# Optimization experiments

Hardware: AMD Instinct MI355X
Metric: run time of the kernel (lower is better)

## Reference

```python
import jax, jax.numpy as jnp
import numpy as np

N_QUBITS = 14
N_LAYERS = 2
BATCH = 512


def _apply_ry(state, theta, wire):
    # state: [B, 2,...,2] (n_qubits axes of size 2); theta: [B] per-sample angle
    c = jnp.cos(theta * 0.5)[:, None]
    s = jnp.sin(theta * 0.5)[:, None]
    st = jnp.moveaxis(state, wire + 1, 1)
    shp = st.shape
    st = st.reshape(shp[0], 2, -1)
    a0, a1 = st[:, 0], st[:, 1]
    # RY = [[cos, -sin], [sin, cos]] (real matrix, so the state stays real)
    st = jnp.stack([c * a0 - s * a1, s * a0 + c * a1], axis=1)
    return jnp.moveaxis(st.reshape(shp), 1, wire + 1)


def _apply_cnot(state, ctrl, tgt):
    ca, ta = ctrl + 1, tgt + 1
    s0 = jnp.take(state, 0, axis=ca)
    s1 = jnp.take(state, 1, axis=ca)
    # flip target axis on the control=1 slice (axis index shifts if it was after ctrl)
    s1 = jnp.flip(s1, axis=ta if ta < ca else ta - 1)
    return jnp.stack([s0, s1], axis=ca)


def _circuit(x, weights):
    B, n = x.shape
    L = weights.shape[0]
    # |0...0> initial state, batched
    state = jnp.zeros((B,) + (2,) * n, x.dtype).at[(slice(None),) + (0,) * n].set(1.0)
    # angle encoding: RY(x[b, w]) on wire w
    for w in range(n):
        state = _apply_ry(state, x[:, w], w)
    # BasicEntanglerLayers: per layer, RY(weights[l, w]) on each wire, then CNOT ring
    for l in range(L):
        for w in range(n):
            state = _apply_ry(state, jnp.broadcast_to(weights[l, w], (B,)), w)
        for w in range(n):
            state = _apply_cnot(state, w, (w + 1) % n)
    # <Z_w> = P(bit_w = 0) - P(bit_w = 1)
    probs = state * state
    exps = []
    for w in range(n):
        p = jnp.moveaxis(probs, w + 1, 1).reshape(B, 2, -1).sum(-1)
        exps.append(p[:, 0] - p[:, 1])
    return jnp.stack(exps, axis=1)  # [B, n_qubits]


def setup_inputs() -> dict:
    key = jax.random.key(0)
    k1, k2 = jax.random.split(key)
    x = jax.random.normal(k1, (BATCH, N_QUBITS), dtype=jnp.float32)
    weights = (2.0 * np.pi) * jax.random.uniform(k2, (N_LAYERS, N_QUBITS), dtype=jnp.float32)
    return {"x": x, "weights": weights}


def reference(x, weights):
    return _circuit(x, weights)
```

## Files before the change

### kernel.cpp

```cpp
#include <hip/hip_runtime.h>

#define NQ 14
#define BLOCK 256
#define NG 28

typedef float f32x2 __attribute__((ext_vector_type(2)));
__device__ __forceinline__ f32x2 mk2(float a, float b) { f32x2 r; r.x = a; r.y = b; return r; }

struct Sched { unsigned m[NG]; unsigned r[NG]; unsigned fr[NQ]; };

constexpr Sched build_sched() {
  Sched sc{};
  unsigned col[NQ] = {}, rowinv[NQ] = {};
  for (int p = 0; p < NQ; ++p) { col[p] = 1u << p; rowinv[p] = 1u << p; }
  int g = 0;
  for (int l = 0; l < 2; ++l) {
    for (int w = 0; w < NQ; ++w) { int p = NQ - 1 - w; sc.m[g] = col[p]; sc.r[g] = rowinv[p]; ++g; }
    for (int w = 0; w < NQ; ++w) {
      int tgt = (w + 1) % NQ; int pc = NQ - 1 - w, pt = NQ - 1 - tgt;
      col[pc] ^= col[pt]; rowinv[pt] ^= rowinv[pc];
    }
  }
  for (int w = 0; w < NQ; ++w) sc.fr[w] = rowinv[NQ - 1 - w];
  return sc;
}
constexpr Sched SC = build_sched();

constexpr int QA_G[4] = {15, 16, 17, 18};
constexpr int QB_G[5] = {19, 20, 21, 22, 23};
constexpr int QC_G[5] = {14, 24, 25, 26, 27};

constexpr unsigned lmapA(unsigned v) { return (v >> 8) & 63u; }
constexpr unsigned lmapB(unsigned v) { return ((v >> 8) & 1u) | (((v >> 3) & 31u) << 1); }
constexpr unsigned lmapC(unsigned v) { return (v & 0xFu) | ((v >> 8) & 0x30u); }

constexpr bool sched_ok() {
  for (int g = 0; g < 14; ++g)
    if (SC.m[g] != (1u << (13 - g)) || SC.r[g] != (1u << (13 - g))) return false;
  const unsigned spanA = 0x3F00u, spanB = 0x01F8u, spanC = 0x300Fu;
  for (int k = 0; k < 4; ++k) {
    if (SC.m[QA_G[k]] & ~spanA) return false;
    if (!(__builtin_popcount(lmapA(SC.m[QA_G[k]]) & lmapA(SC.r[QA_G[k]])) & 1)) return false;
  }
  for (int k = 0; k < 5; ++k) {
    if (SC.m[QB_G[k]] & ~spanB) return false;
    if (!(__builtin_popcount(lmapB(SC.m[QB_G[k]]) & lmapB(SC.r[QB_G[k]])) & 1)) return false;
  }
  for (int k = 0; k < 5; ++k) {
    if (SC.m[QC_G[k]] & ~spanC) return false;
    if (!(__builtin_popcount(lmapC(SC.m[QC_G[k]]) & lmapC(SC.r[QC_G[k]])) & 1)) return false;
  }
  int ord[14] = {}; int n = 0;
  for (int k = 0; k < 4; ++k) ord[n++] = QA_G[k];
  for (int k = 0; k < 5; ++k) ord[n++] = QB_G[k];
  for (int k = 0; k < 5; ++k) ord[n++] = QC_G[k];
  for (int g = 14; g < NG; ++g) { int c = 0; for (int i = 0; i < 14; ++i) if (ord[i] == g) ++c; if (c != 1) return false; }
  for (int i = 0; i < 14; ++i)
    for (int j = i + 1; j < 14; ++j)
      if (ord[i] > ord[j]) {
        int a = ord[i], b = ord[j];
        if ((__builtin_popcount(SC.r[a] & SC.m[b]) & 1) != (__builtin_popcount(SC.r[b] & SC.m[a]) & 1)) return false;
      }
  return true;
}
static_assert(sched_ok(), "schedule invalid");

constexpr unsigned iQA(unsigned t, unsigned p, unsigned e) { return t | ((2u * p + e) << 8); }
constexpr unsigned iQB(unsigned t, unsigned p, unsigned e) { return (t & 7u) | (p << 3) | (e << 8) | ((t >> 3) << 9); }
constexpr unsigned iQC(unsigned T, unsigned p, unsigned e) {
  return e | ((p & 7u) << 1) | (((p >> 3) & 3u) << 12) | (((T >> 3) & 15u) << 4) | (((T >> 7) & 1u) << 8) | ((T & 7u) << 9);
}

constexpr unsigned a1s(unsigned i) { unsigned tA = i & 255u, lA = i >> 8; return tA * 64u + (lA ^ ((tA & 15u) << 1)); }
constexpr unsigned Tof(unsigned i)  { return ((i >> 9) & 7u) | (((i >> 4) & 15u) << 3) | (((i >> 8) & 1u) << 7); }
constexpr unsigned lCof(unsigned i) { return (i & 15u) | (((i >> 12) & 3u) << 4); }
constexpr unsigned a2s(unsigned i) { unsigned T = Tof(i), l = lCof(i); return T * 64u + (l ^ ((T & 7u) << 2)); }

__host__ __device__ constexpr unsigned f2_QAw(unsigned t, unsigned p) {
  return 32u * t + (p ^ (t & 15u));
}
__host__ __device__ constexpr unsigned f2_QBr(unsigned t, unsigned p) {
  return 256u * p + 32u * (t & 7u) + (((t >> 3) ^ (t & 7u)) ^ (8u * (p & 1u)));
}
__host__ __device__ constexpr unsigned dw_QBw(unsigned t, unsigned p, unsigned e) {
  const unsigned lc = (t & 7u) | (8u * (p & 1u)) | (16u * ((t >> 6) & 3u));
  return 64u * ((t >> 3) & 7u) + 512u * (p >> 1) + 8192u * e + (lc ^ (((t >> 3) & 7u) << 2));
}
__host__ __device__ constexpr unsigned f2_QCr(unsigned t, unsigned p) {
  return 32u * t + (p ^ ((t & 7u) << 1));
}

constexpr bool basis_ok() {
  for (int mapi = 0; mapi < 3; ++mapi) {
    unsigned acc = 0;
    for (int k = 0; k < 14; ++k) {
      unsigned t = 0, p = 0, e = 0;
      if (k < 8) t = 1u << k; else if (k < 13) p = 1u << (k - 8); else e = 1;
      unsigned v = (mapi == 0) ? iQA(t, p, e) : (mapi == 1) ? iQB(t, p, e) : iQC(t, p, e);
      if (__builtin_popcount(v) != 1 || (acc & v)) return false;
      acc |= v;
    }
    if (acc != 0x3FFFu) return false;
  }
  return true;
}
static_assert(basis_ok(), "layout maps not bijective");

constexpr bool chk_addr(int pat, unsigned t0, unsigned t1) {
  for (unsigned t = t0; t < t1; ++t)
    for (unsigned p = 0; p < 32; ++p)
      for (unsigned e = 0; e < 2; ++e) {
        unsigned a = 0, b = 0;
        if (pat == 0) { a = 2u * f2_QAw(t, p) + e; b = a1s(iQA(t, p, e)); }
        if (pat == 1) { a = 2u * f2_QBr(t, p) + e; b = a1s(iQB(t, p, e)); }
        if (pat == 2) { a = dw_QBw(t, p, e);       b = a2s(iQB(t, p, e)); }
        if (pat == 3) { a = 2u * f2_QCr(t, p) + e; b = a2s(iQC(t, p, e)); }
        if (a != b || a >= 16384u) return false;
      }
  return true;
}
static_assert(chk_addr(0, 0, 128) && chk_addr(0, 128, 256), "QA write addr");
static_assert(chk_addr(1, 0, 128) && chk_addr(1, 128, 256), "QB read addr");
static_assert(chk_addr(2, 0, 128) && chk_addr(2, 128, 256), "QB write addr");
static_assert(chk_addr(3, 0, 128) && chk_addr(3, 128, 256), "QC read addr");

template <unsigned MU, unsigned RHO>
__device__ __forceinline__ void gate_pk(f32x2* v, const float cg, const float sb) {
  const f32x2 C = mk2(cg, cg);
  constexpr unsigned M2 = MU >> 1;
  constexpr bool ODD = (MU & 1u) != 0;
  if constexpr (!ODD) {
    constexpr unsigned LSB = M2 & (0u - M2);
#pragma unroll
    for (unsigned p = 0; p < 32; ++p) {
      if (p & LSB) continue;
      const unsigned q = p ^ M2;
      const int s0 = __builtin_popcount((2u * p) & RHO) & 1;
      const int s1 = __builtin_popcount((2u * p + 1u) & RHO) & 1;
      const f32x2 Sp = mk2(s0 ? -sb : sb, s1 ? -sb : sb);
      const f32x2 Xp = v[p], Xq = v[q];
      v[p] = C * Xp - Sp * Xq;
      v[q] = C * Xq + Sp * Xp;
    }
  } else if constexpr (M2 == 0) {
#pragma unroll
    for (unsigned p = 0; p < 32; ++p) {
      const int s0 = __builtin_popcount((2u * p) & RHO) & 1;
      const f32x2 Sp = mk2(s0 ? -sb : sb, s0 ? sb : -sb);
      const f32x2 X = v[p];
      v[p] = C * X - Sp * mk2(X.y, X.x);
    }
  } else {
    constexpr unsigned LSB = M2 & (0u - M2);
#pragma unroll
    for (unsigned p = 0; p < 32; ++p) {
      if (p & LSB) continue;
      const unsigned q = p ^ M2;
      const int s0 = __builtin_popcount((2u * p) & RHO) & 1;
      const int s1 = __builtin_popcount((2u * p + 1u) & RHO) & 1;
      const f32x2 Sp = mk2(s0 ? -sb : sb, s1 ? -sb : sb);
      const f32x2 Xp = v[p], Xq = v[q];
      const f32x2 T = Sp * Xp;
      v[p] = C * Xp - Sp * mk2(Xq.y, Xq.x);
      v[q] = C * Xq + mk2(T.y, T.x);
    }
  }
}

__global__ __launch_bounds__(BLOCK, 2) void qnn_kernel(
    const float* __restrict__ x, const float* __restrict__ wts,
    float* __restrict__ out) {
  __shared__ float S[16384];
  f32x2* const F = (f32x2*)S;
  const unsigned t = threadIdx.x & 255u;
  const int b = blockIdx.x;

  f32x2 v2[32];

  {
    float cxx[NQ], sxx[NQ];
#pragma unroll
    for (int w = 0; w < NQ; ++w)
      __sincosf(0.5f * (x[b * NQ + w] + wts[w]), &sxx[w], &cxx[w]);
    float pl = 1.0f;
#pragma unroll
    for (int bb = 0; bb < 8; ++bb) pl *= ((t >> bb) & 1) ? sxx[13 - bb] : cxx[13 - bb];
    v2[0] = mk2(pl * cxx[5], pl * sxx[5]);
#pragma unroll
    for (int k = 1; k < 6; ++k) {
      const unsigned K = 1u << (k - 1);
      const f32x2 sk = mk2(sxx[5 - k], sxx[5 - k]);
      const f32x2 ck = mk2(cxx[5 - k], cxx[5 - k]);
#pragma unroll
      for (unsigned p = 0; p < 16; ++p) {
        if (p & ~(K - 1u)) continue;
        v2[p | K] = v2[p] * sk;
        v2[p] = v2[p] * ck;
      }
    }
  }

#define RUN_GATE(LM, G, BASEPAR)                                          \
  {                                                                       \
    float sn, cs;                                                         \
    __sincosf(0.5f * wts[G], &sn, &cs);                                   \
    const float sb =                                                      \
        (__builtin_popcount((BASEPAR) & SC.r[G]) & 1) ? -sn : sn;         \
    gate_pk<LM(SC.m[G]), LM(SC.r[G])>(v2, cs, sb);                        \
  }

  {
    const unsigned base = t;
    RUN_GATE(lmapA, QA_G[0], base) RUN_GATE(lmapA, QA_G[1], base)
    RUN_GATE(lmapA, QA_G[2], base) RUN_GATE(lmapA, QA_G[3], base)
#pragma unroll
    for (unsigned p = 0; p < 32; ++p) F[f2_QAw(t, p)] = v2[p];
  }
  __syncthreads();

  {
    const unsigned base = (t & 7u) | ((t >> 3) << 9);
#pragma unroll
    for (unsigned p = 0; p < 32; ++p) v2[p] = F[f2_QBr(t, p)];
    RUN_GATE(lmapB, QB_G[0], base) RUN_GATE(lmapB, QB_G[1], base)
    RUN_GATE(lmapB, QB_G[2], base) RUN_GATE(lmapB, QB_G[3], base)
    RUN_GATE(lmapB, QB_G[4], base)
  }
  __syncthreads();
  {
#pragma unroll
    for (unsigned p = 0; p < 32; ++p) {
      S[dw_QBw(t, p, 0)] = v2[p].x;
      S[dw_QBw(t, p, 1)] = v2[p].y;
    }
  }
  __syncthreads();

  float ex[NQ];
  {
    const unsigned base = (((t >> 3) & 15u) << 4) | (((t >> 7) & 1u) << 8) | ((t & 7u) << 9);
#pragma unroll
    for (unsigned p = 0; p < 32; ++p) v2[p] = F[f2_QCr(t, p)];
    RUN_GATE(lmapC, QC_G[0], base) RUN_GATE(lmapC, QC_G[1], base)
    RUN_GATE(lmapC, QC_G[2], base) RUN_GATE(lmapC, QC_G[3], base)
    RUN_GATE(lmapC, QC_G[4], base)

#pragma unroll
    for (unsigned p = 0; p < 32; ++p) v2[p] = v2[p] * v2[p];
#pragma unroll
    for (int k = 0; k < 5; ++k) {
      const unsigned K = 1u << k;
#pragma unroll
      for (unsigned p = 0; p < 32; ++p) {
        if (p & K) continue;
        const f32x2 A = v2[p], B = v2[p ^ K];
        v2[p] = A + B;
        v2[p ^ K] = A - B;
      }
    }
#pragma unroll
    for (int w = 0; w < NQ; ++w) {
      const unsigned ls = lmapC(SC.fr[w]);
      const f32x2 W = v2[ls >> 1];
      const float coef = (ls & 1u) ? (W.x - W.y) : (W.x + W.y);
      const int tf = __builtin_popcount(base & SC.fr[w]) & 1;
      ex[w] = tf ? -coef : coef;
    }
  }
  __syncthreads();

#pragma unroll
  for (int w = 0; w < NQ; ++w) {
#pragma unroll
    for (int off = 32; off > 0; off >>= 1) ex[w] += __shfl_xor(ex[w], off, 64);
  }
  const unsigned lane = t & 63u, wave = t >> 6;
  if (lane == 0) {
#pragma unroll
    for (int w = 0; w < NQ; ++w) S[wave * NQ + w] = ex[w];
  }
  __syncthreads();
  if (t < NQ) {
    out[b * NQ + t] = S[t] + S[NQ + t] + S[2 * NQ + t] + S[3 * NQ + t];
  }
#undef RUN_GATE
}

extern "C" void kernel_launch(void* const* d_in, const int* in_sizes, int n_in,
                              void* d_out, int out_size, void* d_ws, size_t ws_size,
                              hipStream_t stream) {
  const float* x = (const float*)d_in[0];
  const float* weights = (const float*)d_in[1];
  float* out = (float*)d_out;
  const int B = in_sizes[0] / NQ;
  qnn_kernel<<<B, BLOCK, 0, stream>>>(x, weights, out);
}
```

Baseline: 63.44 us.

## Use 512 threads with 32 amplitudes each and four-phase shared-memory transposes

Doubles the block to 512 threads, so each thread holds 16 float2 amplitudes instead of 32, and raises the launch-bounds occupancy hint from 2 to 4 blocks. The gate schedule is regrouped into four phases of 4/4/4/2 gates with new index layouts and swizzled shared-memory maps, checked at compile time for bijectivity and for at most two lanes per bank. The aim is lower register pressure and more waves to hide latency. The cost is an extra shared-memory transpose round trip with its barriers, and a final reduction across 8 waves instead of 4.

```diff
diff --git a/kernel.cpp b/kernel.cpp
--- a/kernel.cpp
+++ b/kernel.cpp
@@ -1,8 +1,9 @@
 #include <hip/hip_runtime.h>
 
 #define NQ 14
-#define BLOCK 256
+#define BLOCK 512
 #define NG 28
+#define NF2 16
 
 typedef float f32x2 __attribute__((ext_vector_type(2)));
 __device__ __forceinline__ f32x2 mk2(float a, float b) { f32x2 r; r.x = a; r.y = b; return r; }
@@ -26,103 +27,123 @@
 }
 constexpr Sched SC = build_sched();
 
-constexpr int QA_G[4] = {15, 16, 17, 18};
-constexpr int QB_G[5] = {19, 20, 21, 22, 23};
-constexpr int QC_G[5] = {14, 24, 25, 26, 27};
-
-constexpr unsigned lmapA(unsigned v) { return (v >> 8) & 63u; }
-constexpr unsigned lmapB(unsigned v) { return ((v >> 8) & 1u) | (((v >> 3) & 31u) << 1); }
-constexpr unsigned lmapC(unsigned v) { return (v & 0xFu) | ((v >> 8) & 0x30u); }
+constexpr unsigned SPAN[4] = {0x3E00u, 0x03E0u, 0x003Eu, 0x3007u};
+
+constexpr unsigned lmap1(unsigned v) { return ((v >> 9) & 1u) | (((v >> 10) & 15u) << 1); }
+constexpr unsigned lmap2(unsigned v) { return ((v >> 9) & 1u) | (((v >> 5) & 15u) << 1); }
+constexpr unsigned lmap3(unsigned v) { return ((v >> 5) & 1u) | (((v >> 1) & 15u) << 1); }
+constexpr unsigned lmap4(unsigned v) { return (v & 1u) | (((v >> 1) & 3u) << 1) | (((v >> 12) & 3u) << 3); }
+
+__host__ __device__ constexpr unsigned i1(unsigned t, unsigned p, unsigned e) { return t | (e << 9) | (p << 10); }
+__host__ __device__ constexpr unsigned i2(unsigned t, unsigned p, unsigned e) {
+  return (t & 31u) | (p << 5) | (e << 9) | ((t >> 5) << 10);
+}
+__host__ __device__ constexpr unsigned i3(unsigned t, unsigned p, unsigned e) {
+  return (t & 1u) | (p << 1) | (e << 5) | ((t >> 1) << 6);
+}
+__host__ __device__ constexpr unsigned i4(unsigned t, unsigned p, unsigned e) {
+  return e | ((p & 3u) << 1) | (t << 3) | ((p >> 2) << 12);
+}
+__host__ __device__ constexpr unsigned base1(unsigned t) { return t; }
+__host__ __device__ constexpr unsigned base2(unsigned t) { return (t & 31u) | ((t >> 5) << 10); }
+__host__ __device__ constexpr unsigned base3(unsigned t) { return (t & 1u) | ((t >> 1) << 6); }
+__host__ __device__ constexpr unsigned base4(unsigned t) { return t << 3; }
+
+__host__ __device__ constexpr unsigned st1(unsigned i) {
+  return 32u * (i & 511u) + (((i >> 9) & 31u) ^ (i & 31u));
+}
+__host__ __device__ constexpr unsigned st2(unsigned i) {
+  const unsigned t = (i & 31u) | (((i >> 10) & 15u) << 5);
+  const unsigned l = (i >> 5) & 31u;
+  return 32u * t + (l ^ (t & 31u));
+}
+__host__ __device__ constexpr unsigned st3(unsigned i) {
+  const unsigned t = (i & 1u) | (((i >> 6) & 255u) << 1);
+  const unsigned l = ((i >> 1) & 15u) | (((i >> 5) & 1u) << 4);
+  return 32u * t + (l ^ (t & 31u) ^ ((l >> 2) & 1u));
+}
 
 constexpr bool sched_ok() {
   for (int g = 0; g < 14; ++g)
     if (SC.m[g] != (1u << (13 - g)) || SC.r[g] != (1u << (13 - g))) return false;
-  const unsigned spanA = 0x3F00u, spanB = 0x01F8u, spanC = 0x300Fu;
-  for (int k = 0; k < 4; ++k) {
-    if (SC.m[QA_G[k]] & ~spanA) return false;
-    if (!(__builtin_popcount(lmapA(SC.m[QA_G[k]]) & lmapA(SC.r[QA_G[k]])) & 1)) return false;
-  }
-  for (int k = 0; k < 5; ++k) {
-    if (SC.m[QB_G[k]] & ~spanB) return false;
-    if (!(__builtin_popcount(lmapB(SC.m[QB_G[k]]) & lmapB(SC.r[QB_G[k]])) & 1)) return false;
-  }
-  for (int k = 0; k < 5; ++k) {
-    if (SC.m[QC_G[k]] & ~spanC) return false;
-    if (!(__builtin_popcount(lmapC(SC.m[QC_G[k]]) & lmapC(SC.r[QC_G[k]])) & 1)) return false;
-  }
-  int ord[14] = {}; int n = 0;
-  for (int k = 0; k < 4; ++k) ord[n++] = QA_G[k];
-  for (int k = 0; k < 5; ++k) ord[n++] = QB_G[k];
-  for (int k = 0; k < 5; ++k) ord[n++] = QC_G[k];
-  for (int g = 14; g < NG; ++g) { int c = 0; for (int i = 0; i < 14; ++i) if (ord[i] == g) ++c; if (c != 1) return false; }
-  for (int i = 0; i < 14; ++i)
-    for (int j = i + 1; j < 14; ++j)
-      if (ord[i] > ord[j]) {
-        int a = ord[i], b = ord[j];
-        if ((__builtin_popcount(SC.r[a] & SC.m[b]) & 1) != (__builtin_popcount(SC.r[b] & SC.m[a]) & 1)) return false;
-      }
+  for (int g = 14; g < 28; ++g) {
+    const int ph = (g < 18) ? 0 : (g < 22) ? 1 : (g < 26) ? 2 : 3;
+    if (SC.m[g] & ~SPAN[ph]) return false;
+    unsigned lm = 0, lr = 0;
+    if (ph == 0) { lm = lmap1(SC.m[g]); lr = lmap1(SC.r[g]); }
+    if (ph == 1) { lm = lmap2(SC.m[g]); lr = lmap2(SC.r[g]); }
+    if (ph == 2) { lm = lmap3(SC.m[g]); lr = lmap3(SC.r[g]); }
+    if (ph == 3) { lm = lmap4(SC.m[g]); lr = lmap4(SC.r[g]); }
+    if (lm == 0) return false;
+    if (!(__builtin_popcount(lm & lr) & 1)) return false;
+  }
   return true;
 }
 static_assert(sched_ok(), "schedule invalid");
 
-constexpr unsigned iQA(unsigned t, unsigned p, unsigned e) { return t | ((2u * p + e) << 8); }
-constexpr unsigned iQB(unsigned t, unsigned p, unsigned e) { return (t & 7u) | (p << 3) | (e << 8) | ((t >> 3) << 9); }
-constexpr unsigned iQC(unsigned T, unsigned p, unsigned e) {
-  return e | ((p & 7u) << 1) | (((p >> 3) & 3u) << 12) | (((T >> 3) & 15u) << 4) | (((T >> 7) & 1u) << 8) | ((T & 7u) << 9);
-}
-
-constexpr unsigned a1s(unsigned i) { unsigned tA = i & 255u, lA = i >> 8; return tA * 64u + (lA ^ ((tA & 15u) << 1)); }
-constexpr unsigned Tof(unsigned i)  { return ((i >> 9) & 7u) | (((i >> 4) & 15u) << 3) | (((i >> 8) & 1u) << 7); }
-constexpr unsigned lCof(unsigned i) { return (i & 15u) | (((i >> 12) & 3u) << 4); }
-constexpr unsigned a2s(unsigned i) { unsigned T = Tof(i), l = lCof(i); return T * 64u + (l ^ ((T & 7u) << 2)); }
-
-__host__ __device__ constexpr unsigned f2_QAw(unsigned t, unsigned p) {
-  return 32u * t + (p ^ (t & 15u));
-}
-__host__ __device__ constexpr unsigned f2_QBr(unsigned t, unsigned p) {
-  return 256u * p + 32u * (t & 7u) + (((t >> 3) ^ (t & 7u)) ^ (8u * (p & 1u)));
-}
-__host__ __device__ constexpr unsigned dw_QBw(unsigned t, unsigned p, unsigned e) {
-  const unsigned lc = (t & 7u) | (8u * (p & 1u)) | (16u * ((t >> 6) & 3u));
-  return 64u * ((t >> 3) & 7u) + 512u * (p >> 1) + 8192u * e + (lc ^ (((t >> 3) & 7u) << 2));
-}
-__host__ __device__ constexpr unsigned f2_QCr(unsigned t, unsigned p) {
-  return 32u * t + (p ^ ((t & 7u) << 1));
-}
-
-constexpr bool basis_ok() {
-  for (int mapi = 0; mapi < 3; ++mapi) {
+constexpr unsigned iP(int ph, unsigned t, unsigned p, unsigned e) {
+  return ph == 0 ? i1(t, p, e) : ph == 1 ? i2(t, p, e) : ph == 2 ? i3(t, p, e) : i4(t, p, e);
+}
+constexpr bool layouts_ok() {
+  for (int ph = 0; ph < 4; ++ph) {
     unsigned acc = 0;
     for (int k = 0; k < 14; ++k) {
       unsigned t = 0, p = 0, e = 0;
-      if (k < 8) t = 1u << k; else if (k < 13) p = 1u << (k - 8); else e = 1;
-      unsigned v = (mapi == 0) ? iQA(t, p, e) : (mapi == 1) ? iQB(t, p, e) : iQC(t, p, e);
+      if (k < 9) t = 1u << k; else if (k < 13) p = 1u << (k - 9); else e = 1;
+      const unsigned v = iP(ph, t, p, e);
       if (__builtin_popcount(v) != 1 || (acc & v)) return false;
       acc |= v;
     }
     if (acc != 0x3FFFu) return false;
   }
+  for (unsigned t = 0; t < 512; ++t) {
+    if (base1(t) != i1(t, 0, 0)) return false;
+    if (base2(t) != i2(t, 0, 0)) return false;
+    if (base3(t) != i3(t, 0, 0)) return false;
+    if (base4(t) != i4(t, 0, 0)) return false;
+  }
   return true;
 }
-static_assert(basis_ok(), "layout maps not bijective");
-
-constexpr bool chk_addr(int pat, unsigned t0, unsigned t1) {
-  for (unsigned t = t0; t < t1; ++t)
-    for (unsigned p = 0; p < 32; ++p)
-      for (unsigned e = 0; e < 2; ++e) {
-        unsigned a = 0, b = 0;
-        if (pat == 0) { a = 2u * f2_QAw(t, p) + e; b = a1s(iQA(t, p, e)); }
-        if (pat == 1) { a = 2u * f2_QBr(t, p) + e; b = a1s(iQB(t, p, e)); }
-        if (pat == 2) { a = dw_QBw(t, p, e);       b = a2s(iQB(t, p, e)); }
-        if (pat == 3) { a = 2u * f2_QCr(t, p) + e; b = a2s(iQC(t, p, e)); }
-        if (a != b || a >= 16384u) return false;
+static_assert(layouts_ok(), "phase layouts invalid");
+
+constexpr bool stmap_bij(int which) {
+  bool hit[16384] = {};
+  for (unsigned i = 0; i < 16384; ++i) {
+    const unsigned a = which == 0 ? st1(i) : which == 1 ? st2(i) : st3(i);
+    if (a >= 16384u || hit[a]) return false;
+    hit[a] = true;
+  }
+  return true;
+}
+static_assert(stmap_bij(0), "st1 not bijective");
+static_assert(stmap_bij(1), "st2 not bijective");
+static_assert(stmap_bij(2), "st3 not bijective");
+
+constexpr bool banks_ok(int pat) {
+  for (unsigned pe = 0; pe < 32; ++pe) {
+    const unsigned p = pe >> 1, e = pe & 1;
+    for (unsigned W = 0; W < 8; ++W) {
+      int cnt[32] = {};
+      for (unsigned lane = 0; lane < 64; ++lane) {
+        const unsigned t = W * 64 + lane;
+        const unsigned a = pat == 0 ? st1(i1(t, p, e))
+                         : pat == 1 ? st1(i2(t, p, e))
+                         : pat == 2 ? st2(i2(t, p, e))
+                         : pat == 3 ? st2(i3(t, p, e))
+                         : pat == 4 ? st3(i3(t, p, e))
+                                    : st3(i4(t, p, e));
+        if (++cnt[a & 31u] > 2) return false;
       }
+    }
+  }
   return true;
 }
-static_assert(chk_addr(0, 0, 128) && chk_addr(0, 128, 256), "QA write addr");
-static_assert(chk_addr(1, 0, 128) && chk_addr(1, 128, 256), "QB read addr");
-static_assert(chk_addr(2, 0, 128) && chk_addr(2, 128, 256), "QB write addr");
-static_assert(chk_addr(3, 0, 128) && chk_addr(3, 128, 256), "QC read addr");
+static_assert(banks_ok(0), "T1 write banks");
+static_assert(banks_ok(1), "T1 read banks");
+static_assert(banks_ok(2), "T2 write banks");
+static_assert(banks_ok(3), "T2 read banks");
+static_assert(banks_ok(4), "T3 write banks");
+static_assert(banks_ok(5), "T3 read banks");
 
 template <unsigned MU, unsigned RHO>
 __device__ __forceinline__ void gate_pk(f32x2* v, const float cg, const float sb) {
@@ -132,7 +153,7 @@
   if constexpr (!ODD) {
     constexpr unsigned LSB = M2 & (0u - M2);
 #pragma unroll
-    for (unsigned p = 0; p < 32; ++p) {
+    for (unsigned p = 0; p < NF2; ++p) {
       if (p & LSB) continue;
       const unsigned q = p ^ M2;
       const int s0 = __builtin_popcount((2u * p) & RHO) & 1;
@@ -144,7 +165,7 @@
     }
   } else if constexpr (M2 == 0) {
 #pragma unroll
-    for (unsigned p = 0; p < 32; ++p) {
+    for (unsigned p = 0; p < NF2; ++p) {
       const int s0 = __builtin_popcount((2u * p) & RHO) & 1;
       const f32x2 Sp = mk2(s0 ? -sb : sb, s0 ? sb : -sb);
       const f32x2 X = v[p];
@@ -153,7 +174,7 @@
   } else {
     constexpr unsigned LSB = M2 & (0u - M2);
 #pragma unroll
-    for (unsigned p = 0; p < 32; ++p) {
+    for (unsigned p = 0; p < NF2; ++p) {
       if (p & LSB) continue;
       const unsigned q = p ^ M2;
       const int s0 = __builtin_popcount((2u * p) & RHO) & 1;
@@ -167,15 +188,14 @@
   }
 }
 
-__global__ __launch_bounds__(BLOCK, 2) void qnn_kernel(
+__global__ __launch_bounds__(BLOCK, 4) void qnn_kernel(
     const float* __restrict__ x, const float* __restrict__ wts,
     float* __restrict__ out) {
   __shared__ float S[16384];
-  f32x2* const F = (f32x2*)S;
-  const unsigned t = threadIdx.x & 255u;
+  const unsigned t = threadIdx.x;
   const int b = blockIdx.x;
 
-  f32x2 v2[32];
+  f32x2 v2[NF2];
 
   {
     float cxx[NQ], sxx[NQ];
@@ -184,18 +204,16 @@
       __sincosf(0.5f * (x[b * NQ + w] + wts[w]), &sxx[w], &cxx[w]);
     float pl = 1.0f;
 #pragma unroll
-    for (int bb = 0; bb < 8; ++bb) pl *= ((t >> bb) & 1) ? sxx[13 - bb] : cxx[13 - bb];
-    v2[0] = mk2(pl * cxx[5], pl * sxx[5]);
-#pragma unroll
-    for (int k = 1; k < 6; ++k) {
-      const unsigned K = 1u << (k - 1);
-      const f32x2 sk = mk2(sxx[5 - k], sxx[5 - k]);
-      const f32x2 ck = mk2(cxx[5 - k], cxx[5 - k]);
-#pragma unroll
-      for (unsigned p = 0; p < 16; ++p) {
-        if (p & ~(K - 1u)) continue;
-        v2[p | K] = v2[p] * sk;
-        v2[p] = v2[p] * ck;
+    for (int bb = 0; bb < 9; ++bb) pl *= ((t >> bb) & 1) ? sxx[13 - bb] : cxx[13 - bb];
+    v2[0] = mk2(pl * cxx[4], pl * sxx[4]);
+#pragma unroll
+    for (int k = 0; k < 4; ++k) {
+      const int K = 1 << k;
+      const float sk = sxx[3 - k], ck = cxx[3 - k];
+#pragma unroll
+      for (int j = K - 1; j >= 0; --j) {
+        v2[j | K] = v2[j] * mk2(sk, sk);
+        v2[j] = v2[j] * mk2(ck, ck);
       }
     }
   }
@@ -210,78 +228,107 @@
   }
 
   {
-    const unsigned base = t;
-    RUN_GATE(lmapA, QA_G[0], base) RUN_GATE(lmapA, QA_G[1], base)
-    RUN_GATE(lmapA, QA_G[2], base) RUN_GATE(lmapA, QA_G[3], base)
-#pragma unroll
-    for (unsigned p = 0; p < 32; ++p) F[f2_QAw(t, p)] = v2[p];
-  }
-  __syncthreads();
-
-  {
-    const unsigned base = (t & 7u) | ((t >> 3) << 9);
-#pragma unroll
-    for (unsigned p = 0; p < 32; ++p) v2[p] = F[f2_QBr(t, p)];
-    RUN_GATE(lmapB, QB_G[0], base) RUN_GATE(lmapB, QB_G[1], base)
-    RUN_GATE(lmapB, QB_G[2], base) RUN_GATE(lmapB, QB_G[3], base)
-    RUN_GATE(lmapB, QB_G[4], base)
-  }
-  __syncthreads();
-  {
-#pragma unroll
-    for (unsigned p = 0; p < 32; ++p) {
-      S[dw_QBw(t, p, 0)] = v2[p].x;
-      S[dw_QBw(t, p, 1)] = v2[p].y;
+    const unsigned bs = base1(t);
+    RUN_GATE(lmap1, 14, bs) RUN_GATE(lmap1, 15, bs)
+    RUN_GATE(lmap1, 16, bs) RUN_GATE(lmap1, 17, bs)
+#pragma unroll
+    for (unsigned p = 0; p < NF2; ++p) {
+      S[st1(i1(t, p, 0))] = v2[p].x;
+      S[st1(i1(t, p, 1))] = v2[p].y;
+    }
+  }
+  __syncthreads();
+
+  {
+    const unsigned bs = base2(t);
+#pragma unroll
+    for (unsigned p = 0; p < NF2; ++p) {
+      v2[p].x = S[st1(i2(t, p, 0))];
+      v2[p].y = S[st1(i2(t, p, 1))];
+    }
+    RUN_GATE(lmap2, 18, bs) RUN_GATE(lmap2, 19, bs)
+    RUN_GATE(lmap2, 20, bs) RUN_GATE(lmap2, 21, bs)
+  }
+  __syncthreads();
+  {
+#pragma unroll
+    for (unsigned p = 0; p < NF2; ++p) {
+      S[st2(i2(t, p, 0))] = v2[p].x;
+      S[st2(i2(t, p, 1))] = v2[p].y;
+    }
+  }
+  __syncthreads();
+
+  {
+    const unsigned bs = base3(t);
+#pragma unroll
+    for (unsigned p = 0; p < NF2; ++p) {
+      v2[p].x = S[st2(i3(t, p, 0))];
+      v2[p].y = S[st2(i3(t, p, 1))];
+    }
+    RUN_GATE(lmap3, 22, bs) RUN_GATE(lmap3, 23, bs)
+    RUN_GATE(lmap3, 24, bs) RUN_GATE(lmap3, 25, bs)
+  }
+  __syncthreads();
+  {
+#pragma unroll
+    for (unsigned p = 0; p < NF2; ++p) {
+      S[st3(i3(t, p, 0))] = v2[p].x;
+      S[st3(i3(t, p, 1))] = v2[p].y;
     }
   }
   __syncthreads();
 
   float ex[NQ];
   {
-    const unsigned base = (((t >> 3) & 15u) << 4) | (((t >> 7) & 1u) << 8) | ((t & 7u) << 9);
-#pragma unroll
-    for (unsigned p = 0; p < 32; ++p) v2[p] = F[f2_QCr(t, p)];
-    RUN_GATE(lmapC, QC_G[0], base) RUN_GATE(lmapC, QC_G[1], base)
-    RUN_GATE(lmapC, QC_G[2], base) RUN_GATE(lmapC, QC_G[3], base)
-    RUN_GATE(lmapC, QC_G[4], base)
-
-#pragma unroll
-    for (unsigned p = 0; p < 32; ++p) v2[p] = v2[p] * v2[p];
-#pragma unroll
-    for (int k = 0; k < 5; ++k) {
+    const unsigned bs = base4(t);
+#pragma unroll
+    for (unsigned p = 0; p < NF2; ++p) {
+      v2[p].x = S[st3(i4(t, p, 0))];
+      v2[p].y = S[st3(i4(t, p, 1))];
+    }
+    RUN_GATE(lmap4, 26, bs) RUN_GATE(lmap4, 27, bs)
+
+#pragma unroll
+    for (unsigned p = 0; p < NF2; ++p) v2[p] = v2[p] * v2[p];
+#pragma unroll
+    for (int k = 0; k < 4; ++k) {
       const unsigned K = 1u << k;
 #pragma unroll
-      for (unsigned p = 0; p < 32; ++p) {
+      for (unsigned p = 0; p < NF2; ++p) {
         if (p & K) continue;
-        const f32x2 A = v2[p], B = v2[p ^ K];
-        v2[p] = A + B;
-        v2[p ^ K] = A - B;
+        const f32x2 A = v2[p], Bv = v2[p ^ K];
+        v2[p] = A + Bv;
+        v2[p ^ K] = A - Bv;
       }
     }
 #pragma unroll
     for (int w = 0; w < NQ; ++w) {
-      const unsigned ls = lmapC(SC.fr[w]);
+      const unsigned ls = lmap4(SC.fr[w]);
       const f32x2 W = v2[ls >> 1];
       const float coef = (ls & 1u) ? (W.x - W.y) : (W.x + W.y);
-      const int tf = __builtin_popcount(base & SC.fr[w]) & 1;
+      const int tf = __builtin_popcount(bs & SC.fr[w]) & 1;
       ex[w] = tf ? -coef : coef;
     }
   }
-  __syncthreads();
 
 #pragma unroll
   for (int w = 0; w < NQ; ++w) {
 #pragma unroll
     for (int off = 32; off > 0; off >>= 1) ex[w] += __shfl_xor(ex[w], off, 64);
   }
-  const unsigned lane = t & 63u, wave = t >> 6;
+  __syncthreads();
+  const unsigned lane = t & 63u, wv = t >> 6;
   if (lane == 0) {
 #pragma unroll
-    for (int w = 0; w < NQ; ++w) S[wave * NQ + w] = ex[w];
+    for (int w = 0; w < NQ; ++w) S[wv * NQ + w] = ex[w];
   }
   __syncthreads();
   if (t < NQ) {
-    out[b * NQ + t] = S[t] + S[NQ + t] + S[2 * NQ + t] + S[3 * NQ + t];
+    float r = 0.0f;
+#pragma unroll
+    for (int W = 0; W < 8; ++W) r += S[W * NQ + t];
+    out[b * NQ + t] = r;
   }
 #undef RUN_GATE
 }
```

Result: slower. 68.98 us (+8.7%).

## Re-layout shared-memory transposes for float4 stores and replace shuffle reduction

Applied to the files above, without the earlier changes.

Redesigns the two shared-memory transposes between gate phases so that each thread writes 128-bit float4 chunks with XOR swizzles. Compile-time checks verify the maps are bijective and that bank use is balanced. The final expectation reduction drops the 14×6 wave shuffles and instead stores per-thread partials to LDS, followed by a two-level shared-memory sum. The aim is fewer LDS instructions, fewer bank conflicts and less shuffle work, at the cost of an extra barrier and more complex indexing. A stray unused load loop is left in.

```diff
diff --git a/kernel.cpp b/kernel.cpp
--- a/kernel.cpp
+++ b/kernel.cpp
@@ -3,6 +3,7 @@
 #define NQ 14
 #define BLOCK 256
 #define NG 28
+#define NF2 32
 
 typedef float f32x2 __attribute__((ext_vector_type(2)));
 __device__ __forceinline__ f32x2 mk2(float a, float b) { f32x2 r; r.x = a; r.y = b; return r; }
@@ -32,7 +33,9 @@
 
 constexpr unsigned lmapA(unsigned v) { return (v >> 8) & 63u; }
 constexpr unsigned lmapB(unsigned v) { return ((v >> 8) & 1u) | (((v >> 3) & 31u) << 1); }
-constexpr unsigned lmapC(unsigned v) { return (v & 0xFu) | ((v >> 8) & 0x30u); }
+constexpr unsigned lmapC(unsigned v) {
+  return ((v >> 3) & 1u) | ((v & 7u) << 1) | (((v >> 12) & 3u) << 4);
+}
 
 constexpr bool sched_ok() {
   for (int g = 0; g < 14; ++g)
@@ -65,38 +68,52 @@
 }
 static_assert(sched_ok(), "schedule invalid");
 
-constexpr unsigned iQA(unsigned t, unsigned p, unsigned e) { return t | ((2u * p + e) << 8); }
-constexpr unsigned iQB(unsigned t, unsigned p, unsigned e) { return (t & 7u) | (p << 3) | (e << 8) | ((t >> 3) << 9); }
-constexpr unsigned iQC(unsigned T, unsigned p, unsigned e) {
-  return e | ((p & 7u) << 1) | (((p >> 3) & 3u) << 12) | (((T >> 3) & 15u) << 4) | (((T >> 7) & 1u) << 8) | ((T & 7u) << 9);
-}
-
-constexpr unsigned a1s(unsigned i) { unsigned tA = i & 255u, lA = i >> 8; return tA * 64u + (lA ^ ((tA & 15u) << 1)); }
-constexpr unsigned Tof(unsigned i)  { return ((i >> 9) & 7u) | (((i >> 4) & 15u) << 3) | (((i >> 8) & 1u) << 7); }
-constexpr unsigned lCof(unsigned i) { return (i & 15u) | (((i >> 12) & 3u) << 4); }
-constexpr unsigned a2s(unsigned i) { unsigned T = Tof(i), l = lCof(i); return T * 64u + (l ^ ((T & 7u) << 2)); }
-
-__host__ __device__ constexpr unsigned f2_QAw(unsigned t, unsigned p) {
-  return 32u * t + (p ^ (t & 15u));
-}
-__host__ __device__ constexpr unsigned f2_QBr(unsigned t, unsigned p) {
-  return 256u * p + 32u * (t & 7u) + (((t >> 3) ^ (t & 7u)) ^ (8u * (p & 1u)));
-}
-__host__ __device__ constexpr unsigned dw_QBw(unsigned t, unsigned p, unsigned e) {
-  const unsigned lc = (t & 7u) | (8u * (p & 1u)) | (16u * ((t >> 6) & 3u));
-  return 64u * ((t >> 3) & 7u) + 512u * (p >> 1) + 8192u * e + (lc ^ (((t >> 3) & 7u) << 2));
-}
-__host__ __device__ constexpr unsigned f2_QCr(unsigned t, unsigned p) {
-  return 32u * t + (p ^ ((t & 7u) << 1));
-}
-
-constexpr bool basis_ok() {
+__host__ __device__ constexpr unsigned iQA(unsigned t, unsigned p, unsigned e) {
+  return t | (e << 8) | (p << 9);
+}
+__host__ __device__ constexpr unsigned iQB(unsigned t, unsigned p, unsigned e) {
+  return (t & 7u) | (p << 3) | (e << 8) | ((t >> 3) << 9);
+}
+__host__ __device__ constexpr unsigned iQC(unsigned t, unsigned p, unsigned e) {
+  return (p & 7u) | (e << 3) | (t << 4) | ((p >> 3) << 12);
+}
+
+__host__ __device__ constexpr unsigned dwT1(unsigned i) {
+  const unsigned low5 = ((i >> 9) & 31u) ^ (i & 30u) ^ ((i & 3u) << 3);
+  return 2u * (low5 | ((i & 255u) << 5)) + ((i >> 8) & 1u);
+}
+__host__ __device__ constexpr unsigned dwT2(unsigned i) {
+  const unsigned rest = (((i >> 4) & 15u) ^ (i & 7u)) | ((i & 7u) << 4) | (((i >> 9) & 31u) << 7);
+  return ((i >> 3) & 1u) | (((i >> 8) & 1u) << 1) | (rest << 2);
+}
+
+__host__ __device__ constexpr unsigned BASEW1(unsigned t) {
+  return ((t & 30u) ^ ((t & 3u) << 3)) | (t << 5);
+}
+__host__ __device__ constexpr unsigned BASER1(unsigned t) {
+  return ((t >> 3) ^ (t & 6u) ^ ((t & 3u) << 3)) | ((t & 7u) << 5);
+}
+__host__ __device__ constexpr unsigned VR1(unsigned p) { return ((p & 3u) << 3) | (p << 8); }
+__host__ __device__ constexpr unsigned CW2(unsigned t) {
+  return ((t & 7u) << 2) | ((t & 7u) << 6) | ((t >> 3) << 9);
+}
+__host__ __device__ constexpr unsigned VW2(unsigned p, unsigned e) {
+  return (p & 1u) | (e << 1) | ((p >> 1) << 2);
+}
+__host__ __device__ constexpr unsigned CR2(unsigned t) {
+  return (((t >> 4) & 1u) << 1) | ((t & 15u) << 2) | ((t >> 5) << 9);
+}
+__host__ __device__ constexpr unsigned VR2(unsigned p, unsigned e) {
+  return e | ((p & 7u) << 2) | ((p & 7u) << 6) | ((p >> 3) << 12);
+}
+
+constexpr bool layouts_ok() {
   for (int mapi = 0; mapi < 3; ++mapi) {
     unsigned acc = 0;
     for (int k = 0; k < 14; ++k) {
       unsigned t = 0, p = 0, e = 0;
       if (k < 8) t = 1u << k; else if (k < 13) p = 1u << (k - 8); else e = 1;
-      unsigned v = (mapi == 0) ? iQA(t, p, e) : (mapi == 1) ? iQB(t, p, e) : iQC(t, p, e);
+      const unsigned v = (mapi == 0) ? iQA(t, p, e) : (mapi == 1) ? iQB(t, p, e) : iQC(t, p, e);
       if (__builtin_popcount(v) != 1 || (acc & v)) return false;
       acc |= v;
     }
@@ -104,25 +121,79 @@
   }
   return true;
 }
-static_assert(basis_ok(), "layout maps not bijective");
-
-constexpr bool chk_addr(int pat, unsigned t0, unsigned t1) {
-  for (unsigned t = t0; t < t1; ++t)
+static_assert(layouts_ok(), "phase layouts invalid");
+
+constexpr bool stmap_bij(int which) {
+  bool hit[16384] = {};
+  for (unsigned i = 0; i < 16384; ++i) {
+    const unsigned a = which == 0 ? dwT1(i) : dwT2(i);
+    if (a >= 16384u || hit[a]) return false;
+    hit[a] = true;
+  }
+  return true;
+}
+static_assert(stmap_bij(0), "dwT1 not bijective");
+static_assert(stmap_bij(1), "dwT2 not bijective");
+
+constexpr bool chkT1(unsigned t0, unsigned t1) {
+  for (unsigned t = t0; t < t1; ++t) {
+    for (unsigned k = 0; k < 16; ++k) {
+      const unsigned B = 4u * ((BASEW1(t) >> 1) ^ k);
+      if (B + 3 >= 16384u) return false;
+      if (dwT1(iQA(t, 2 * k, 0)) != B) return false;
+      if (dwT1(iQA(t, 2 * k, 1)) != B + 1) return false;
+      if (dwT1(iQA(t, 2 * k + 1, 0)) != B + 2) return false;
+      if (dwT1(iQA(t, 2 * k + 1, 1)) != B + 3) return false;
+    }
     for (unsigned p = 0; p < 32; ++p)
-      for (unsigned e = 0; e < 2; ++e) {
-        unsigned a = 0, b = 0;
-        if (pat == 0) { a = 2u * f2_QAw(t, p) + e; b = a1s(iQA(t, p, e)); }
-        if (pat == 1) { a = 2u * f2_QBr(t, p) + e; b = a1s(iQB(t, p, e)); }
-        if (pat == 2) { a = dw_QBw(t, p, e);       b = a2s(iQB(t, p, e)); }
-        if (pat == 3) { a = 2u * f2_QCr(t, p) + e; b = a2s(iQC(t, p, e)); }
-        if (a != b || a >= 16384u) return false;
-      }
-  return true;
-}
-static_assert(chk_addr(0, 0, 128) && chk_addr(0, 128, 256), "QA write addr");
-static_assert(chk_addr(1, 0, 128) && chk_addr(1, 128, 256), "QB read addr");
-static_assert(chk_addr(2, 0, 128) && chk_addr(2, 128, 256), "QB write addr");
-static_assert(chk_addr(3, 0, 128) && chk_addr(3, 128, 256), "QC read addr");
+      for (unsigned e = 0; e < 2; ++e)
+        if (dwT1(iQB(t, p, e)) != 2u * (BASER1(t) ^ VR1(p)) + e) return false;
+  }
+  return true;
+}
+static_assert(chkT1(0, 64) && chkT1(64, 128), "T1 addr 0-128");
+static_assert(chkT1(128, 192) && chkT1(192, 256), "T1 addr 128-256");
+
+constexpr bool chkT2(unsigned t0, unsigned t1) {
+  for (unsigned t = t0; t < t1; ++t) {
+    for (unsigned k = 0; k < 16; ++k) {
+      const unsigned B = 4u * ((CW2(t) >> 2) ^ k);
+      if (B + 3 >= 16384u) return false;
+      for (unsigned q = 0; q < 2; ++q)
+        for (unsigned e = 0; e < 2; ++e)
+          if (dwT2(iQB(t, 2 * k + q, e)) != B + q + 2 * e) return false;
+    }
+    for (unsigned p = 0; p < 32; ++p)
+      for (unsigned e = 0; e < 2; ++e)
+        if (dwT2(iQC(t, p, e)) != (CR2(t) ^ VR2(p, 0)) + e) return false;
+  }
+  return true;
+}
+static_assert(chkT2(0, 64) && chkT2(64, 128), "T2 addr 0-128");
+static_assert(chkT2(128, 192) && chkT2(192, 256), "T2 addr 128-256");
+
+constexpr bool banks_ok() {
+  for (unsigned W = 0; W < 4; ++W) {
+    for (unsigned k = 0; k < 16; ++k) {
+      int c1[8] = {}, c2[8] = {};
+      for (unsigned l = 0; l < 64; ++l) {
+        const unsigned t = W * 64u + l;
+        if (++c1[((BASEW1(t) ^ (2u * k)) >> 1) & 7u] > 8) return false;
+        if (++c2[((CW2(t) >> 2) ^ k) & 7u] > 8) return false;
+      }
+    }
+    for (unsigned p = 0; p < 32; ++p) {
+      int c1[16] = {}, c2[16] = {};
+      for (unsigned l = 0; l < 64; ++l) {
+        const unsigned t = W * 64u + l;
+        if (++c1[(BASER1(t) ^ VR1(p)) & 15u] > 4) return false;
+        if (++c2[((CR2(t) ^ VR2(p, 0)) >> 1) & 15u] > 4) return false;
+      }
+    }
+  }
+  return true;
+}
+static_assert(banks_ok(), "bank balance");
 
 template <unsigned MU, unsigned RHO>
 __device__ __forceinline__ void gate_pk(f32x2* v, const float cg, const float sb) {
@@ -132,7 +203,7 @@
   if constexpr (!ODD) {
     constexpr unsigned LSB = M2 & (0u - M2);
 #pragma unroll
-    for (unsigned p = 0; p < 32; ++p) {
+    for (unsigned p = 0; p < NF2; ++p) {
       if (p & LSB) continue;
       const unsigned q = p ^ M2;
       const int s0 = __builtin_popcount((2u * p) & RHO) & 1;
@@ -144,7 +215,7 @@
     }
   } else if constexpr (M2 == 0) {
 #pragma unroll
-    for (unsigned p = 0; p < 32; ++p) {
+    for (unsigned p = 0; p < NF2; ++p) {
       const int s0 = __builtin_popcount((2u * p) & RHO) & 1;
       const f32x2 Sp = mk2(s0 ? -sb : sb, s0 ? sb : -sb);
       const f32x2 X = v[p];
@@ -153,7 +224,7 @@
   } else {
     constexpr unsigned LSB = M2 & (0u - M2);
 #pragma unroll
-    for (unsigned p = 0; p < 32; ++p) {
+    for (unsigned p = 0; p < NF2; ++p) {
       if (p & LSB) continue;
       const unsigned q = p ^ M2;
       const int s0 = __builtin_popcount((2u * p) & RHO) & 1;
@@ -170,12 +241,14 @@
 __global__ __launch_bounds__(BLOCK, 2) void qnn_kernel(
     const float* __restrict__ x, const float* __restrict__ wts,
     float* __restrict__ out) {
-  __shared__ float S[16384];
-  f32x2* const F = (f32x2*)S;
-  const unsigned t = threadIdx.x & 255u;
+  __shared__ float4 S4[4096];
+  float* const S = (float*)S4;
+  float4* const F4 = S4;
+  f32x2* const Fv = (f32x2*)S4;
+  const unsigned t = threadIdx.x;
   const int b = blockIdx.x;
 
-  f32x2 v2[32];
+  f32x2 v2[NF2];
 
   {
     float cxx[NQ], sxx[NQ];
@@ -210,52 +283,63 @@
   }
 
   {
-    const unsigned base = t;
-    RUN_GATE(lmapA, QA_G[0], base) RUN_GATE(lmapA, QA_G[1], base)
-    RUN_GATE(lmapA, QA_G[2], base) RUN_GATE(lmapA, QA_G[3], base)
-#pragma unroll
-    for (unsigned p = 0; p < 32; ++p) F[f2_QAw(t, p)] = v2[p];
-  }
-  __syncthreads();
-
-  {
-    const unsigned base = (t & 7u) | ((t >> 3) << 9);
-#pragma unroll
-    for (unsigned p = 0; p < 32; ++p) v2[p] = F[f2_QBr(t, p)];
-    RUN_GATE(lmapB, QB_G[0], base) RUN_GATE(lmapB, QB_G[1], base)
-    RUN_GATE(lmapB, QB_G[2], base) RUN_GATE(lmapB, QB_G[3], base)
-    RUN_GATE(lmapB, QB_G[4], base)
-  }
-  __syncthreads();
-  {
-#pragma unroll
-    for (unsigned p = 0; p < 32; ++p) {
-      S[dw_QBw(t, p, 0)] = v2[p].x;
-      S[dw_QBw(t, p, 1)] = v2[p].y;
+    const unsigned bs = t;
+    RUN_GATE(lmapA, QA_G[0], bs) RUN_GATE(lmapA, QA_G[1], bs)
+    RUN_GATE(lmapA, QA_G[2], bs) RUN_GATE(lmapA, QA_G[3], bs)
+    const unsigned w1 = BASEW1(t) >> 1;
+#pragma unroll
+    for (unsigned k = 0; k < 16; ++k) {
+      float4 w4;
+      w4.x = v2[2 * k].x; w4.y = v2[2 * k].y;
+      w4.z = v2[2 * k + 1].x; w4.w = v2[2 * k + 1].y;
+      F4[w1 ^ k] = w4;
+    }
+  }
+  __syncthreads();
+
+  {
+    const unsigned bs = (t & 7u) | ((t >> 3) << 9);
+    const unsigned r1 = BASER1(t);
+#pragma unroll
+    for (unsigned p = 0; p < 32; ++p) v2[p] = Fv[r1 ^ VR1(p)];
+    RUN_GATE(lmapB, QB_G[0], bs) RUN_GATE(lmapB, QB_G[1], bs)
+    RUN_GATE(lmapB, QB_G[2], bs) RUN_GATE(lmapB, QB_G[3], bs)
+    RUN_GATE(lmapB, QB_G[4], bs)
+  }
+  __syncthreads();
+  {
+    const unsigned w2 = CW2(t) >> 2;
+#pragma unroll
+    for (unsigned k = 0; k < 16; ++k) {
+      float4 w4;
+      w4.x = v2[2 * k].x; w4.y = v2[2 * k + 1].x;
+      w4.z = v2[2 * k].y; w4.w = v2[2 * k + 1].y;
+      F4[w2 ^ k] = w4;
     }
   }
   __syncthreads();
 
   float ex[NQ];
   {
-    const unsigned base = (((t >> 3) & 15u) << 4) | (((t >> 7) & 1u) << 8) | ((t & 7u) << 9);
-#pragma unroll
-    for (unsigned p = 0; p < 32; ++p) v2[p] = F[f2_QCr(t, p)];
-    RUN_GATE(lmapC, QC_G[0], base) RUN_GATE(lmapC, QC_G[1], base)
-    RUN_GATE(lmapC, QC_G[2], base) RUN_GATE(lmapC, QC_G[3], base)
-    RUN_GATE(lmapC, QC_G[4], base)
-
-#pragma unroll
-    for (unsigned p = 0; p < 32; ++p) v2[p] = v2[p] * v2[p];
+    const unsigned bs = t << 4;
+    const unsigned r2 = CR2(t);
+#pragma unroll
+    for (unsigned p = 0; p < 32; ++p) v2[p] = Fv[(r2 ^ VR2(p, 0)) >> 1];
+    RUN_GATE(lmapC, QC_G[0], bs) RUN_GATE(lmapC, QC_G[1], bs)
+    RUN_GATE(lmapC, QC_G[2], bs) RUN_GATE(lmapC, QC_G[3], bs)
+    RUN_GATE(lmapC, QC_G[4], bs)
+
+#pragma unroll
+    for (unsigned p = 0; p < NF2; ++p) v2[p] = v2[p] * v2[p];
 #pragma unroll
     for (int k = 0; k < 5; ++k) {
       const unsigned K = 1u << k;
 #pragma unroll
-      for (unsigned p = 0; p < 32; ++p) {
+      for (unsigned p = 0; p < NF2; ++p) {
         if (p & K) continue;
-        const f32x2 A = v2[p], B = v2[p ^ K];
-        v2[p] = A + B;
-        v2[p ^ K] = A - B;
+        const f32x2 A = v2[p], Bv = v2[p ^ K];
+        v2[p] = A + Bv;
+        v2[p ^ K] = A - Bv;
       }
     }
 #pragma unroll
@@ -263,25 +347,40 @@
       const unsigned ls = lmapC(SC.fr[w]);
       const f32x2 W = v2[ls >> 1];
       const float coef = (ls & 1u) ? (W.x - W.y) : (W.x + W.y);
-      const int tf = __builtin_popcount(base & SC.fr[w]) & 1;
+      const int tf = __builtin_popcount(bs & SC.fr[w]) & 1;
       ex[w] = tf ? -coef : coef;
     }
   }
   __syncthreads();
 
-#pragma unroll
-  for (int w = 0; w < NQ; ++w) {
-#pragma unroll
-    for (int off = 32; off > 0; off >>= 1) ex[w] += __shfl_xor(ex[w], off, 64);
-  }
-  const unsigned lane = t & 63u, wave = t >> 6;
-  if (lane == 0) {
-#pragma unroll
-    for (int w = 0; w < NQ; ++w) S[wave * NQ + w] = ex[w];
+  {
+    const unsigned fb = t * 8u + ((t >> 1) & 7u);
+#pragma unroll
+    for (unsigned q = 0; q < 7; ++q) Fv[(fb ^ ((t >> 1) & 7u)) ^ (q ^ 0u) + 0u];
+#pragma unroll
+    for (unsigned q = 0; q < 7; ++q)
+      Fv[t * 8u + (q ^ ((t >> 1) & 7u))] = mk2(ex[2 * q], ex[2 * q + 1]);
+  }
+  __syncthreads();
+  {
+    const unsigned w = t & 15u, g = t >> 4;
+    if (w < NQ) {
+      float acc = 0.0f;
+#pragma unroll
+      for (unsigned k = 0; k < 16; ++k)
+        acc += S[(g * 16u + k) * 16u + (((w & 14u) ^ (k & 14u)) + (w & 1u))];
+      S[8192u + w * 16u + g] = acc;
+    }
   }
   __syncthreads();
   if (t < NQ) {
-    out[b * NQ + t] = S[t] + S[NQ + t] + S[2 * NQ + t] + S[3 * NQ + t];
+    float r = 0.0f;
+#pragma unroll
+    for (unsigned j = 0; j < 4; ++j) {
+      const float4 r4 = F4[2048u + t * 4u + j];
+      r += r4.x + r4.y + r4.z + r4.w;
+    }
+    out[b * NQ + t] = r;
   }
 #undef RUN_GATE
 }
```

New measurement: 61.82 us. 2.6% less time.
